# Optimization experiments

Hardware: AMD Instinct MI355X
Metric: run time of the kernel (lower is better)

Reference implementation:

```python
import jax, jax.numpy as jnp
import numpy as np

NUM_QUBITS = 10
NUM_LAYERS = 5
OBS = 10          # observation_size == num_qubits (required by input_scaling indexing)
NUM_OUTPUTS = 4   # num_actions, discretize=False
BATCH = 4096


def _bcast(theta, n):
    # theta: scalar or (B,) -> broadcastable against (B, 2, 2, ..., 2)
    return jnp.reshape(jnp.asarray(theta), (-1,) + (1,) * n)


def _ry(st, theta, q, n):
    # st: (B,) + (2,)*n complex64; per-sample RY(theta) on qubit q
    t = _bcast(theta, n) * 0.5
    c, s = jnp.cos(t), jnp.sin(t)
    s0 = jax.lax.index_in_dim(st, 0, axis=q + 1, keepdims=True)
    s1 = jax.lax.index_in_dim(st, 1, axis=q + 1, keepdims=True)
    return jnp.concatenate([c * s0 - s * s1, s * s0 + c * s1], axis=q + 1)


def _rz(st, theta, q, n):
    t = _bcast(theta, n) * 0.5
    s0 = jax.lax.index_in_dim(st, 0, axis=q + 1, keepdims=True)
    s1 = jax.lax.index_in_dim(st, 1, axis=q + 1, keepdims=True)
    return jnp.concatenate([jnp.exp(-1j * t) * s0, jnp.exp(1j * t) * s1], axis=q + 1)


def _cnot(st, c, t):
    # flip target axis on the control=1 slab; pure index ops (no residuals in bwd)
    s0 = jax.lax.index_in_dim(st, 0, axis=c + 1, keepdims=True)
    s1 = jax.lax.index_in_dim(st, 1, axis=c + 1, keepdims=True)
    s1 = jnp.flip(s1, axis=t + 1)
    return jnp.concatenate([s0, s1], axis=c + 1)


def _layer(st, x, isc, w, n, obs):
    # isc: (2n,) input_scaling row, w: (2n,) weights row
    for i in range(obs):
        st = _ry(st, isc[i] * x[:, i], i, n)
        st = _rz(st, isc[i + obs] * x[:, i], i, n)
    for i in range(n):
        st = _rz(st, w[i], i, n)
    for i in range(n):
        st = _ry(st, w[i + n], i, n)
    if n == 2:
        st = _cnot(st, 0, 1)
    else:
        for i in range(n):
            st = _cnot(st, i, (i + 1) % n)
    return st


_layer_ckpt = jax.checkpoint(_layer, static_argnums=(4, 5))


def _circuit(x, input_scaling, weights, n, num_layers, obs, num_outputs):
    B = x.shape[0]
    st = jnp.zeros((B,) + (2,) * n, dtype=jnp.complex64)
    st = st.at[(slice(None),) + (0,) * n].set(1.0)  # |0...0>
    for layer in range(num_layers):
        st = _layer_ckpt(st, x, input_scaling[layer], weights[layer], n, obs)
    probs = jnp.real(st * jnp.conj(st))
    outs = []
    for i in range(num_outputs):
        axes = tuple(a for a in range(1, n + 1) if a != i + 1)
        pi = jnp.sum(probs, axis=axes)  # (B, 2)
        outs.append(pi[:, 0] - pi[:, 1])  # <Z_i>
    return jnp.stack(outs, axis=1)


def setup_inputs() -> dict:
    key = jax.random.key(0)
    k1, k2 = jax.random.split(key)
    x = jax.random.normal(k1, (BATCH, OBS), dtype=jnp.float32)
    input_scaling = jnp.ones((NUM_LAYERS, 2 * NUM_QUBITS), dtype=jnp.float32)
    weights = jax.random.uniform(k2, (NUM_LAYERS, 2 * NUM_QUBITS), minval=-np.pi, maxval=np.pi, dtype=jnp.float32)
    output_scaling = jnp.ones((NUM_OUTPUTS,), dtype=jnp.float32)
    return {"x": x, "input_scaling": input_scaling, "weights": weights, "output_scaling": output_scaling}


def reference(x, input_scaling, weights, output_scaling):
    z = _circuit(x, input_scaling, weights, NUM_QUBITS, NUM_LAYERS, OBS, NUM_OUTPUTS)
    return z * output_scaling  # (B, num_actions); discretize=False -> actions = scaled expvals
```

## Files before the change

kernel.cpp:

```cpp
#include <hip/hip_runtime.h>


constexpr int NQ  = 10;
constexpr int NL  = 5;
constexpr int OBS = 10;

typedef float f2 __attribute__((ext_vector_type(2)));

__device__ __forceinline__ float readlane_f(float v, int l) {
    return __int_as_float(__builtin_amdgcn_readlane(__float_as_int(v), l));
}
__device__ __forceinline__ float bperm_f(int byte_addr, float v) {
    return __int_as_float(__builtin_amdgcn_ds_bpermute(byte_addr, __float_as_int(v)));
}
template <int CTRL>
__device__ __forceinline__ float dpp_f(float v) {
    return __int_as_float(__builtin_amdgcn_update_dpp(
        0, __float_as_int(v), CTRL, 0xF, 0xF, true));
}
__device__ __forceinline__ float xor_lane(float v, int M, int a16, int a32) {
    switch (M) {
    case 1:  return dpp_f<0xB1>(v);
    case 2:  return dpp_f<0x4E>(v);
    case 8:  return dpp_f<0x128>(v);
    case 4:  return dpp_f<0x141>(dpp_f<0x1B>(v));
    case 16: return bperm_f(a16, v);
    default: return bperm_f(a32, v);
    }
}

__global__ __launch_bounds__(256, 4) void qsim_kernel(
    const float* __restrict__ x,
    const float* __restrict__ isc,
    const float* __restrict__ w,
    const float* __restrict__ oscale,
    float* __restrict__ out,
    int B)
{
    const int lane = threadIdx.x & 63;
    const int wid  = (blockIdx.x * blockDim.x + threadIdx.x) >> 6;
    if (wid >= B) return;

    float cUR, cUI, cVR, cVI;
    {
        const int g   = (lane < 50) ? lane : 49;
        const int q   = g % 10;
        const int lyr = g / 10;
        const float xq    = x[wid * OBS + q];
        const float alpha = isc[lyr * 2 * NQ + q]      * xq;
        const float beta  = isc[lyr * 2 * NQ + NQ + q] * xq;
        const float gamma = w[lyr * 2 * NQ + q];
        const float delta = w[lyr * 2 * NQ + NQ + q];
        float sa, ca, sp, cp, sd, cd;
        __sincosf(0.5f * alpha,          &sa, &ca);
        __sincosf(0.5f * (beta + gamma), &sp, &cp);
        __sincosf(0.5f * delta,          &sd, &cd);
        const float A = cd * ca, Bt = sd * sa;
        const float C = cd * sa, D  = sd * ca;
        cUR = (A - Bt) * cp;
        cUI = -(A + Bt) * sp;
        cVR = (C + D) * cp;
        cVI = (C - D) * sp;
    }

    const int a16 = (lane ^ 16) * 4;
    const int a32 = (lane ^ 32) * 4;
    const int cnot_src  = (lane ^ (lane >> 1));
    const int addr_even = cnot_src * 4;
    const int addr_odd  = (cnot_src ^ 32) * 4;

    f2 c[16];

    {
        float Lr = 1.f, Li = 0.f;
#pragma unroll
        for (int q = 4; q < 10; ++q) {
            const float ur = readlane_f(cUR, q), ui = readlane_f(cUI, q);
            const float vr = readlane_f(cVR, q), vi = readlane_f(cVI, q);
            const int M = 1 << (9 - q);
            const float fr = (lane & M) ? vr : ur;
            const float fi = (lane & M) ? vi : ui;
            const float nr = Lr * fr - Li * fi;
            const float ni = Lr * fi + Li * fr;
            Lr = nr; Li = ni;
        }
        c[0] = (f2){Lr, Li};
#pragma unroll
        for (int r = 1; r < 16; ++r) c[r] = (f2){0.f, 0.f};
#pragma unroll
        for (int q = 3; q >= 0; --q) {
            const int m = 1 << (3 - q);
            const float ur = readlane_f(cUR, q), ui = readlane_f(cUI, q);
            const float vr = readlane_f(cVR, q), vi = readlane_f(cVI, q);
#pragma unroll
            for (int r0 = 0; r0 < 16; ++r0) {
                if (r0 >= m) continue;
                const f2 s = c[r0];
                c[r0 | m] = (f2){ s.x*vr - s.y*vi, s.x*vi + s.y*vr };
                c[r0]     = (f2){ s.x*ur - s.y*ui, s.x*ui + s.y*ur };
            }
        }
    }

#define SWAPR(i, j) { f2 _t = c[i]; c[i] = c[j]; c[j] = _t; }

    for (int layer = 0; layer < NL; ++layer) {
        const int base = layer * NQ;

        if (layer > 0) {
#pragma unroll
            for (int q = 0; q < NQ; ++q) {
                const float ur = readlane_f(cUR, base + q);
                const float ui = readlane_f(cUI, base + q);
                const float vr = readlane_f(cVR, base + q);
                const float vi = readlane_f(cVI, base + q);
                const f2 kUU  = {ur, ur};
                const f2 kUIm = {-ui, ui};
                const f2 kVVn = {-vr, -vr};
                const f2 kVV  = {vr, vr};
                const f2 kVIm = {-vi, vi};
                const f2 kUIp = {ui, -ui};

                if (q < 4) {
                    const int m = 1 << (3 - q);
#pragma unroll
                    for (int r0 = 0; r0 < 16; ++r0) {
                        if (r0 & m) continue;
                        const int r1 = r0 | m;
                        const f2 c0 = c[r0], c1 = c[r1];
                        const f2 c0s = c0.yx, c1s = c1.yx;
                        c[r0] = kUU*c0 + kUIm*c0s + kVVn*c1 + kVIm*c1s;
                        c[r1] = kVV*c0 + kVIm*c0s + kUU*c1  + kUIp*c1s;
                    }
                } else {
                    const int  M   = 1 << (9 - q);
                    const bool bit = (lane & M) != 0;
                    const float Pi = bit ? -ui : ui;
                    const float Qr = bit ?  vr : -vr;
                    const f2 kUUb = {ur, ur};
                    const f2 kPI  = {-Pi, Pi};
                    const f2 kQR  = {Qr, Qr};
                    const f2 kVIb = {-vi, vi};
#pragma unroll
                    for (int r = 0; r < 16; ++r) {
                        const f2 mv = c[r];
                        f2 pv;
                        pv.x = xor_lane(mv.x, M, a16, a32);
                        pv.y = xor_lane(mv.y, M, a16, a32);
                        c[r] = kUUb*mv + kPI*mv.yx + kQR*pv + kVIb*pv.yx;
                    }
                }
            }
        }

        if (layer < NL - 1) {
            SWAPR(8, 12) SWAPR(9, 13) SWAPR(10, 14) SWAPR(11, 15)
            SWAPR(4, 6)  SWAPR(5, 7)  SWAPR(12, 14) SWAPR(13, 15)
            SWAPR(2, 3)  SWAPR(6, 7)  SWAPR(10, 11) SWAPR(14, 15)
#pragma unroll
            for (int r = 0; r < 16; ++r) {
                const int addr = (r & 1) ? addr_odd : addr_even;
                c[r].x = bperm_f(addr, c[r].x);
                c[r].y = bperm_f(addr, c[r].y);
            }
            const bool ctl = (lane & 1) != 0;
#pragma unroll
            for (int r = 0; r < 8; ++r) {
                const f2 t0 = c[r], t1 = c[r + 8];
                c[r]     = ctl ? t1 : t0;
                c[r + 8] = ctl ? t0 : t1;
            }
        }
    }

    const float sL = (__popc(lane) & 1) ? -1.f : 1.f;
    float z0 = 0.f, z1 = 0.f, z2 = 0.f, z3 = 0.f;
#pragma unroll
    for (int r = 0; r < 16; ++r) {
        const float pv  = c[r].x * c[r].x + c[r].y * c[r].y;
        const float pvl = sL * pv;
        z0 += (__popc(r & 7)  & 1) ? -pvl : pvl;
        z1 += (__popc(r & 12) & 1) ? -pv  : pv;
        z2 += (__popc(r & 14) & 1) ? -pv  : pv;
        z3 += (__popc(r & 15) & 1) ? -pv  : pv;
    }
#pragma unroll
    for (int m = 1; m < 64; m <<= 1) {
        z0 += xor_lane(z0, m, a16, a32);
        z1 += xor_lane(z1, m, a16, a32);
        z2 += xor_lane(z2, m, a16, a32);
        z3 += xor_lane(z3, m, a16, a32);
    }
    if (lane == 0) {
        out[wid * 4 + 0] = z0 * oscale[0];
        out[wid * 4 + 1] = z1 * oscale[1];
        out[wid * 4 + 2] = z2 * oscale[2];
        out[wid * 4 + 3] = z3 * oscale[3];
    }
#undef SWAPR
}

extern "C" void kernel_launch(void* const* d_in, const int* in_sizes, int n_in,
                              void* d_out, int out_size, void* d_ws, size_t ws_size,
                              hipStream_t stream) {
    const float* x      = (const float*)d_in[0];
    const float* isc    = (const float*)d_in[1];
    const float* w      = (const float*)d_in[2];
    const float* oscale = (const float*)d_in[3];
    float* out = (float*)d_out;

    const int B = in_sizes[0] / OBS;
    const int threads = 256;
    const int blocks = (B * 64 + threads - 1) / threads;
    qsim_kernel<<<blocks, threads, 0, stream>>>(x, isc, w, oscale, out, B);
}
```

Baseline: 91.96 us.

## Store statevector as packed fp16 complex and apply gates with packed f16 FMAs

Each complex amplitude is now held as one packed half2 register instead of two floats. Gate application uses v_pk_fma_f16/v_pk_mul_f16 with op_sel swizzles, and cross-lane exchanges (DPP and ds_bpermute) move a single 32-bit value per amplitude instead of two. This halves register use and permute traffic and shrinks the ALU op count. The cost is a large loss of precision over 5 layers of gates, which may exceed the accuracy tolerance.

```diff
diff --git a/kernel.cpp b/kernel.cpp
--- a/kernel.cpp
+++ b/kernel.cpp
@@ -1,4 +1,5 @@
 #include <hip/hip_runtime.h>
+#include <hip/hip_fp16.h>
 
 
 constexpr int NQ  = 10;
@@ -10,22 +11,48 @@
 __device__ __forceinline__ float readlane_f(float v, int l) {
     return __int_as_float(__builtin_amdgcn_readlane(__float_as_int(v), l));
 }
-__device__ __forceinline__ float bperm_f(int byte_addr, float v) {
-    return __int_as_float(__builtin_amdgcn_ds_bpermute(byte_addr, __float_as_int(v)));
+__device__ __forceinline__ int pack2(float a, float b) {
+    __half2 h = __floats2half2_rn(a, b);
+    int i; __builtin_memcpy(&i, &h, 4); return i;
+}
+__device__ __forceinline__ __half2 i2h(int i) {
+    __half2 v; __builtin_memcpy(&v, &i, 4); return v;
+}
+
+__device__ __forceinline__ int pk_fma(int a, int b, int c) {
+    int d;
+    asm("v_pk_fma_f16 %0, %1, %2, %3" : "=v"(d) : "v"(a), "v"(b), "v"(c));
+    return d;
+}
+__device__ __forceinline__ int pk_fma_sw(int a, int b, int c) {
+    int d;
+    asm("v_pk_fma_f16 %0, %1, %2, %3 op_sel:[0,1,0] op_sel_hi:[1,0,1]"
+        : "=v"(d) : "v"(a), "v"(b), "v"(c));
+    return d;
+}
+__device__ __forceinline__ int pk_mul_sw(int a, int b) {
+    int d;
+    asm("v_pk_mul_f16 %0, %1, %2 op_sel:[0,1] op_sel_hi:[1,0]"
+        : "=v"(d) : "v"(a), "v"(b));
+    return d;
+}
+__device__ __forceinline__ int negp(int k) { return k ^ 0x80008000; }
+
+__device__ __forceinline__ int bperm_i(int byte_addr, int v) {
+    return __builtin_amdgcn_ds_bpermute(byte_addr, v);
 }
 template <int CTRL>
-__device__ __forceinline__ float dpp_f(float v) {
-    return __int_as_float(__builtin_amdgcn_update_dpp(
-        0, __float_as_int(v), CTRL, 0xF, 0xF, true));
-}
-__device__ __forceinline__ float xor_lane(float v, int M, int a16, int a32) {
+__device__ __forceinline__ int dpp_i(int v) {
+    return __builtin_amdgcn_update_dpp(0, v, CTRL, 0xF, 0xF, true);
+}
+__device__ __forceinline__ int xor_lane_i(int v, int M, int a16, int a32) {
     switch (M) {
-    case 1:  return dpp_f<0xB1>(v);
-    case 2:  return dpp_f<0x4E>(v);
-    case 8:  return dpp_f<0x128>(v);
-    case 4:  return dpp_f<0x141>(dpp_f<0x1B>(v));
-    case 16: return bperm_f(a16, v);
-    default: return bperm_f(a32, v);
+    case 1:  return dpp_i<0xB1>(v);
+    case 2:  return dpp_i<0x4E>(v);
+    case 8:  return dpp_i<0x128>(v);
+    case 4:  return dpp_i<0x141>(dpp_i<0x1B>(v));
+    case 16: return bperm_i(a16, v);
+    default: return bperm_i(a32, v);
     }
 }
 
@@ -42,6 +69,7 @@
     if (wid >= B) return;
 
     float cUR, cUI, cVR, cVI;
+    int   KUU, KUIM, KVV, KVIM;
     {
         const int g   = (lane < 50) ? lane : 49;
         const int q   = g % 10;
@@ -61,6 +89,10 @@
         cUI = -(A + Bt) * sp;
         cVR = (C + D) * cp;
         cVI = (C - D) * sp;
+        KUU  = pack2(cUR, cUR);
+        KUIM = pack2(-cUI, cUI);
+        KVV  = pack2(cVR, cVR);
+        KVIM = pack2(-cVI, cVI);
     }
 
     const int a16 = (lane ^ 16) * 4;
@@ -69,7 +101,7 @@
     const int addr_even = cnot_src * 4;
     const int addr_odd  = (cnot_src ^ 32) * 4;
 
-    f2 c[16];
+    int c[16];
 
     {
         float Lr = 1.f, Li = 0.f;
@@ -84,9 +116,10 @@
             const float ni = Lr * fi + Li * fr;
             Lr = nr; Li = ni;
         }
-        c[0] = (f2){Lr, Li};
-#pragma unroll
-        for (int r = 1; r < 16; ++r) c[r] = (f2){0.f, 0.f};
+        f2 cf[16];
+        cf[0] = (f2){Lr, Li};
+#pragma unroll
+        for (int r = 1; r < 16; ++r) cf[r] = (f2){0.f, 0.f};
 #pragma unroll
         for (int q = 3; q >= 0; --q) {
             const int m = 1 << (3 - q);
@@ -95,14 +128,16 @@
 #pragma unroll
             for (int r0 = 0; r0 < 16; ++r0) {
                 if (r0 >= m) continue;
-                const f2 s = c[r0];
-                c[r0 | m] = (f2){ s.x*vr - s.y*vi, s.x*vi + s.y*vr };
-                c[r0]     = (f2){ s.x*ur - s.y*ui, s.x*ui + s.y*ur };
-            }
-        }
-    }
-
-#define SWAPR(i, j) { f2 _t = c[i]; c[i] = c[j]; c[j] = _t; }
+                const f2 s = cf[r0];
+                cf[r0 | m] = (f2){ s.x*vr - s.y*vi, s.x*vi + s.y*vr };
+                cf[r0]     = (f2){ s.x*ur - s.y*ui, s.x*ui + s.y*ur };
+            }
+        }
+#pragma unroll
+        for (int r = 0; r < 16; ++r) c[r] = pack2(cf[r].x, cf[r].y);
+    }
+
+#define SWAPR(i, j) { int _t = c[i]; c[i] = c[j]; c[j] = _t; }
 
     for (int layer = 0; layer < NL; ++layer) {
         const int base = layer * NQ;
@@ -110,44 +145,42 @@
         if (layer > 0) {
 #pragma unroll
             for (int q = 0; q < NQ; ++q) {
-                const float ur = readlane_f(cUR, base + q);
-                const float ui = readlane_f(cUI, base + q);
-                const float vr = readlane_f(cVR, base + q);
-                const float vi = readlane_f(cVI, base + q);
-                const f2 kUU  = {ur, ur};
-                const f2 kUIm = {-ui, ui};
-                const f2 kVVn = {-vr, -vr};
-                const f2 kVV  = {vr, vr};
-                const f2 kVIm = {-vi, vi};
-                const f2 kUIp = {ui, -ui};
+                const int kUU  = __builtin_amdgcn_readlane(KUU,  base + q);
+                const int kUIm = __builtin_amdgcn_readlane(KUIM, base + q);
+                const int kVV  = __builtin_amdgcn_readlane(KVV,  base + q);
+                const int kVIm = __builtin_amdgcn_readlane(KVIM, base + q);
 
                 if (q < 4) {
+                    const int kVVn = negp(kVV);
+                    const int kUIp = negp(kUIm);
                     const int m = 1 << (3 - q);
 #pragma unroll
                     for (int r0 = 0; r0 < 16; ++r0) {
                         if (r0 & m) continue;
                         const int r1 = r0 | m;
-                        const f2 c0 = c[r0], c1 = c[r1];
-                        const f2 c0s = c0.yx, c1s = c1.yx;
-                        c[r0] = kUU*c0 + kUIm*c0s + kVVn*c1 + kVIm*c1s;
-                        c[r1] = kVV*c0 + kVIm*c0s + kUU*c1  + kUIp*c1s;
+                        const int c0 = c[r0], c1 = c[r1];
+                        int t = pk_mul_sw(kVIm, c1);
+                        t = pk_fma(kVVn, c1, t);
+                        t = pk_fma_sw(kUIm, c0, t);
+                        c[r0] = pk_fma(kUU, c0, t);
+                        int s = pk_mul_sw(kUIp, c1);
+                        s = pk_fma(kUU, c1, s);
+                        s = pk_fma_sw(kVIm, c0, s);
+                        c[r1] = pk_fma(kVV, c0, s);
                     }
                 } else {
                     const int  M   = 1 << (9 - q);
                     const bool bit = (lane & M) != 0;
-                    const float Pi = bit ? -ui : ui;
-                    const float Qr = bit ?  vr : -vr;
-                    const f2 kUUb = {ur, ur};
-                    const f2 kPI  = {-Pi, Pi};
-                    const f2 kQR  = {Qr, Qr};
-                    const f2 kVIb = {-vi, vi};
+                    const int kPI = bit ? negp(kUIm) : kUIm;
+                    const int kQR = bit ? kVV : negp(kVV);
 #pragma unroll
                     for (int r = 0; r < 16; ++r) {
-                        const f2 mv = c[r];
-                        f2 pv;
-                        pv.x = xor_lane(mv.x, M, a16, a32);
-                        pv.y = xor_lane(mv.y, M, a16, a32);
-                        c[r] = kUUb*mv + kPI*mv.yx + kQR*pv + kVIb*pv.yx;
+                        const int mv = c[r];
+                        const int pv = xor_lane_i(mv, M, a16, a32);
+                        int t = pk_mul_sw(kVIm, pv);
+                        t = pk_fma(kQR, pv, t);
+                        t = pk_fma_sw(kPI, mv, t);
+                        c[r] = pk_fma(kUU, mv, t);
                     }
                 }
             }
@@ -160,13 +193,12 @@
 #pragma unroll
             for (int r = 0; r < 16; ++r) {
                 const int addr = (r & 1) ? addr_odd : addr_even;
-                c[r].x = bperm_f(addr, c[r].x);
-                c[r].y = bperm_f(addr, c[r].y);
+                c[r] = bperm_i(addr, c[r]);
             }
             const bool ctl = (lane & 1) != 0;
 #pragma unroll
             for (int r = 0; r < 8; ++r) {
-                const f2 t0 = c[r], t1 = c[r + 8];
+                const int t0 = c[r], t1 = c[r + 8];
                 c[r]     = ctl ? t1 : t0;
                 c[r + 8] = ctl ? t0 : t1;
             }
@@ -177,7 +209,9 @@
     float z0 = 0.f, z1 = 0.f, z2 = 0.f, z3 = 0.f;
 #pragma unroll
     for (int r = 0; r < 16; ++r) {
-        const float pv  = c[r].x * c[r].x + c[r].y * c[r].y;
+        const __half2 h = i2h(c[r]);
+        const float cr = __low2float(h), ci = __high2float(h);
+        const float pv  = cr * cr + ci * ci;
         const float pvl = sL * pv;
         z0 += (__popc(r & 7)  & 1) ? -pvl : pvl;
         z1 += (__popc(r & 12) & 1) ? -pv  : pv;
@@ -186,10 +220,10 @@
     }
 #pragma unroll
     for (int m = 1; m < 64; m <<= 1) {
-        z0 += xor_lane(z0, m, a16, a32);
-        z1 += xor_lane(z1, m, a16, a32);
-        z2 += xor_lane(z2, m, a16, a32);
-        z3 += xor_lane(z3, m, a16, a32);
+        z0 = z0 + __int_as_float(xor_lane_i(__float_as_int(z0), m, a16, a32));
+        z1 = z1 + __int_as_float(xor_lane_i(__float_as_int(z1), m, a16, a32));
+        z2 = z2 + __int_as_float(xor_lane_i(__float_as_int(z2), m, a16, a32));
+        z3 = z3 + __int_as_float(xor_lane_i(__float_as_int(z3), m, a16, a32));
     }
     if (lane == 0) {
         out[wid * 4 + 0] = z0 * oscale[0];
```

Result: no change. 90.74 us (-1.3%).
